# Kernel optimization log

Measured on AMD Instinct MI355X. Metric: run time of the kernel, lower is better.

## Reference

```python
import jax, jax.numpy as jnp
import numpy as np

B, S, D = 2, 2048, 1024
H, HD = 16, 64          # num_heads, head_dim
K = 32                  # JL n_components


def setup_inputs() -> dict:
    key = jax.random.key(0)
    k1, k2, k3, k4 = jax.random.split(key, 4)
    return {
        "hidden_states": jax.random.normal(k1, (B, S, D), dtype=jnp.float32),
        "W_attn": jax.random.normal(k2, (D, 3 * D), dtype=jnp.float32) * 0.02,
        "b_attn": jnp.zeros((3 * D,), dtype=jnp.float32),
        "S_proj": jax.random.normal(k3, (K, HD), dtype=jnp.float32) / np.sqrt(K),
        "W_proj": jax.random.normal(k4, (D, D), dtype=jnp.float32) * 0.02,
        "b_proj": jnp.zeros((D,), dtype=jnp.float32),
    }


def reference(hidden_states, W_attn, b_attn, S_proj, W_proj, b_proj):
    b, s, d = hidden_states.shape
    # GPT2 Conv1D: x @ W + b, then split into q,k,v
    qkv = hidden_states @ W_attn + b_attn            # [B,S,3D]
    q, k, v = jnp.split(qkv, 3, axis=-1)
    # split heads -> [B,H,S,HD]
    def split_heads(x):
        return x.reshape(b, s, H, HD).transpose(0, 2, 1, 3)
    q = split_heads(q) @ S_proj.T                    # [B,H,S,K] JL-reduced
    k = split_heads(k) @ S_proj.T                    # [B,H,S,K]
    v = split_heads(v)                               # [B,H,S,HD]
    # naive attention: scale by sqrt(value head_dim) per GPT2 _attn
    scores = jnp.einsum("bhqk,bhsk->bhqs", q, k) / jnp.sqrt(
        jnp.asarray(HD, dtype=v.dtype))              # [B,H,S,S]
    causal = jnp.tril(jnp.ones((s, s), dtype=bool))
    mask_value = jnp.finfo(scores.dtype).min
    scores = jnp.where(causal, scores, mask_value)
    attn = jax.nn.softmax(scores, axis=-1)
    out = jnp.einsum("bhqs,bhsd->bhqd", attn, v)     # [B,H,S,HD]
    out = out.transpose(0, 2, 1, 3).reshape(b, s, d)  # merge heads
    return out @ W_proj + b_proj
```

## Files before the change

### kernel.cpp

```cpp
#include <hip/hip_runtime.h>
#include <hip/hip_bf16.h>
#include <stdint.h>

#define B_ 2
#define S_ 2048
#define D_ 1024
#define H_ 16
#define HD_ 64
#define KJL 32
#define N3 3072
#define N2 2048

typedef __attribute__((ext_vector_type(8))) __bf16 bf16x8;
typedef __attribute__((ext_vector_type(4))) float floatx4;
typedef __attribute__((ext_vector_type(4))) short short4v;
typedef __attribute__((ext_vector_type(2))) unsigned int uint2v;

__device__ __forceinline__ unsigned short f2b(float x) {
  union { float f; unsigned u; } v; v.f = x;
  unsigned r = v.u + 0x7fffu + ((v.u >> 16) & 1u);
  return (unsigned short)(r >> 16);
}

__device__ __forceinline__ unsigned int pkbf(float lo, float hi) {
  union { float f; unsigned u; } a, b;
  a.f = lo; b.f = hi;
  return __builtin_amdgcn_perm(b.u + 0x8000u, a.u + 0x8000u, 0x07060302u);
}

__device__ __forceinline__ void async16(const void* g, void* l) {
  __builtin_amdgcn_global_load_lds((__attribute__((address_space(1))) void*)(g),
                                   (__attribute__((address_space(3))) void*)(l),
                                   16, 0, 0);
}

__global__ __launch_bounds__(256)
void prep_kernel(const float* __restrict__ hidden, unsigned short* __restrict__ hB,
                 const float* __restrict__ W_attn, const float* __restrict__ b_attn,
                 const float* __restrict__ Sp, const float* __restrict__ W_proj,
                 unsigned short* __restrict__ Bt2, unsigned short* __restrict__ WpT,
                 float* __restrict__ bias2) {
  __shared__ float shmem[2048];
  const int bid = blockIdx.x;
  const int tid = threadIdx.x;

  if (bid < 512) {
    const int n4 = (B_ * S_ * D_) / 4;
    int i = bid * 256 + tid;
    for (; i < n4; i += 512 * 256) {
      float4 v = *(const float4*)(hidden + 4 * (size_t)i);
      short4v o = {(short)f2b(v.x), (short)f2b(v.y), (short)f2b(v.z), (short)f2b(v.w)};
      *(short4v*)(hB + 4 * (size_t)i) = o;
    }
  } else if (bid < 2560) {
    const float* in;
    unsigned short* out;
    int Cs, local;
    if (bid < 1536) { local = bid - 512;  in = W_attn + 2048; out = Bt2 + 1024 * 1024; Cs = N3; }
    else            { local = bid - 1536; in = W_proj;        out = WpT;               Cs = D_; }
    float (*t)[33] = (float(*)[33])shmem;
    int c0 = (local & 31) * 32, r0 = (local >> 5) * 32;
    int tx = tid & 31, ty = tid >> 5;
    for (int j = 0; j < 32; j += 8)
      t[ty + j][tx] = in[(size_t)(r0 + ty + j) * Cs + c0 + tx];
    __syncthreads();
    for (int j = 0; j < 32; j += 8)
      out[(size_t)(c0 + ty + j) * D_ + r0 + tx] = f2b(t[tx][ty + j]);
  } else {
    const int lb = bid - 2560;
    const int part = lb >> 6;
    const int h = (lb >> 2) & 15;
    const int dc = lb & 3;
    for (int i = tid; i < 32 * 64; i += 256) shmem[i] = Sp[i];
    __syncthreads();
    const float scale = part ? 1.0f : 0.125f * 1.44269504f;
    const int d = dc * 256 + tid;
    float w[64];
    const float* src = W_attn + (size_t)d * N3 + part * D_ + h * 64;
    for (int j = 0; j < 16; ++j) {
      float4 v = *(const float4*)&src[j * 4];
      w[j * 4 + 0] = v.x; w[j * 4 + 1] = v.y; w[j * 4 + 2] = v.z; w[j * 4 + 3] = v.w;
    }
    const int nbase = part * 512 + h * 32;
    for (int kjl = 0; kjl < 32; ++kjl) {
      float acc = 0.f;
      for (int hd = 0; hd < 64; ++hd) acc += w[hd] * shmem[kjl * 64 + hd];
      Bt2[(size_t)(nbase + kjl) * D_ + d] = f2b(acc * scale);
    }
    if (dc == 0 && tid < 32) {
      float acc = 0.f;
      for (int hd = 0; hd < 64; ++hd) acc += b_attn[part * D_ + h * 64 + hd] * shmem[tid * 64 + hd];
      bias2[nbase + tid] = acc * scale;
    }
  }
}

__global__ __launch_bounds__(256, 2)
void qkv2_gemm_kernel(const unsigned short* __restrict__ A,
                      const unsigned short* __restrict__ Bt,
                      const float* __restrict__ b_attn,
                      const float* __restrict__ bias2,
                      unsigned short* __restrict__ Qjl,
                      unsigned short* __restrict__ Kjl,
                      unsigned short* __restrict__ Vc) {
  __shared__ __align__(16) unsigned short As[2][128 * 32];
  __shared__ __align__(16) unsigned short Bs[2][128 * 32];
  const int tid = threadIdx.x;
  const int lane = tid & 63, wv = tid >> 6;
  const int quad = lane >> 4, col = lane & 15;
  const int wm = wv >> 1, wn = wv & 1;
  const int m0 = blockIdx.y * 128, n0 = blockIdx.x * 128;

  floatx4 acc[4][4] = {};

  for (int kk = 0; kk < D_; kk += 64) {
    for (int it = 0; it < 4; ++it) {
      int c = it * 256 + tid;
      int ks = c >> 9, row = (c >> 2) & 127, kc = c & 3;
      async16(A + (size_t)(m0 + row) * D_ + kk + ks * 32 + kc * 8,
              (unsigned short*)As + c * 8);
    }
    for (int it = 0; it < 4; ++it) {
      int c = it * 256 + tid;
      int ks = c >> 9, row = (c >> 2) & 127, kc = c & 3;
      async16(Bt + (size_t)(n0 + row) * D_ + kk + ks * 32 + kc * 8,
              (unsigned short*)Bs + c * 8);
    }
    asm volatile("s_waitcnt vmcnt(0)" ::: "memory");
    __syncthreads();
    for (int ks = 0; ks < 2; ++ks) {
      bf16x8 af[4], bfr[4];
      for (int mt = 0; mt < 4; ++mt)
        af[mt] = *(const bf16x8*)&As[ks][(wm * 64 + mt * 16 + col) * 32 + quad * 8];
      for (int nt = 0; nt < 4; ++nt)
        bfr[nt] = *(const bf16x8*)&Bs[ks][(wn * 64 + nt * 16 + col) * 32 + quad * 8];
      for (int mt = 0; mt < 4; ++mt)
        for (int nt = 0; nt < 4; ++nt)
          acc[mt][nt] = __builtin_amdgcn_mfma_f32_16x16x32_bf16(
              af[mt], bfr[nt], acc[mt][nt], 0, 0, 0);
    }
    __syncthreads();
  }

  const int pq = n0 >> 9;
  for (int mt = 0; mt < 4; ++mt) {
    int gm0 = m0 + wm * 64 + mt * 16 + quad * 4;
    int b = gm0 >> 11, s = gm0 & (S_ - 1);
    for (int nt = 0; nt < 4; ++nt) {
      int gn = n0 + wn * 64 + nt * 16 + col;
      if (pq >= 2) {
        int vcol = gn - 1024;
        float bs = b_attn[2048 + vcol];
        int h = vcol >> 6, hd = vcol & 63;
        short4v vv;
        for (int i = 0; i < 4; ++i)
          vv[i] = (short)f2b(acc[mt][nt][i] + bs);
        size_t idx = ((((size_t)(b * H_ + h) * 64 + (s >> 5)) * 64 + hd) * 32 + (s & 31));
        *(short4v*)&Vc[idx] = vv;
      } else {
        float bs = bias2[gn];
        int gl = gn & 511;
        int h = gl >> 5, kjl = gl & 31;
        unsigned short* dst = pq ? Kjl : Qjl;
        size_t base = ((size_t)(b * H_ + h) * S_ + s) * KJL + kjl;
        for (int i = 0; i < 4; ++i)
          dst[base + (size_t)i * KJL] = f2b(acc[mt][nt][i] + bs);
      }
    }
  }
}

__global__ __launch_bounds__(512, 1)
void attn_kernel(const unsigned short* __restrict__ Qjl,
                 const unsigned short* __restrict__ Kjl,
                 const unsigned short* __restrict__ Vc,
                 unsigned short* __restrict__ AO) {
  __shared__ __align__(16) unsigned short Kb[3][4096];
  __shared__ __align__(16) unsigned short Vb[3][8192];
  __shared__ __align__(16) unsigned short Ps[8][2048];
  const int tid = threadIdx.x;
  const int lane = tid & 63, wv = tid >> 6;
  const int quad = lane >> 4, l15 = lane & 15;

  const int blk = blockIdx.x;
  const int bh = blk & 31;
  const int u = blk >> 5;
  const int b = bh >> 4, h = bh & 15;

  const unsigned short* Kg = Kjl + (size_t)bh * S_ * KJL;
  const unsigned short* Vg = Vc + (size_t)bh * (64 * 64 * 32);

  char* Pw = (char*)&Ps[wv][0];
  const int pswz = l15 << 4;
  const floatx4 zz = {0.f, 0.f, 0.f, 0.f};

#define STAGE(bu, c) do {                                                   \
    const char* ks_ = (const char*)(Kg + (size_t)(c) * 4096);               \
    const char* vs_ = (const char*)(Vg + (size_t)(c) * 8192);               \
    char* kd_ = (char*)&Kb[bu][0];                                          \
    char* vd_ = (char*)&Vb[bu][0];                                          \
    async16(ks_ + tid * 16,        kd_ + tid * 16);                         \
    async16(vs_ + tid * 16,        vd_ + tid * 16);                         \
    async16(vs_ + tid * 16 + 8192, vd_ + tid * 16 + 8192);                  \
  } while (0)

  for (int ph = 0; ph < 2; ++ph) {
    const int g = ph ? (15 - u) : u;
    const int t = g * 8 + wv;
    const int nch = g + 1;
    const int lastc = g;

    bf16x8 aq = *(const bf16x8*)&Qjl[(size_t)(bh * S_ + t * 16 + l15) * KJL + quad * 8];

    floatx4 o[4] = {};
    floatx4 psum = {};

    STAGE(0, 0);
    if (nch > 1) {
      STAGE(1, 1);
      asm volatile("s_waitcnt vmcnt(3)" ::: "memory");
    } else {
      asm volatile("s_waitcnt vmcnt(0)" ::: "memory");
    }
    __builtin_amdgcn_s_barrier();

    for (int kt = 0; kt < nch; ++kt) {
      const int cur = kt % 3;
      if (kt + 2 < nch) STAGE((kt + 2) % 3, kt + 2);

      const char* Kc = (const char*)&Kb[cur][0];
      const char* Vl = (const char*)&Vb[cur][0];

      bf16x8 ak[8];
      for (int sm = 0; sm < 8; ++sm)
        ak[sm] = *(const bf16x8*)(Kc + (sm * 16 + l15) * 64 + quad * 16);

      floatx4 sc[8];
      __builtin_amdgcn_s_setprio(1);
      for (int sm = 0; sm < 8; ++sm)
        sc[sm] = __builtin_amdgcn_mfma_f32_16x16x32_bf16(ak[sm], aq, zz, 0, 0, 0);
      __builtin_amdgcn_s_setprio(0);

      if (kt == lastc) {
        int qloc = wv * 16 + l15;
        for (int sm = 0; sm < 8; ++sm)
          for (int i = 0; i < 4; ++i)
            if (sm * 16 + quad * 4 + i > qloc) sc[sm][i] = -1e30f;
      }

      for (int sm = 0; sm < 8; ++sm) {
        float p0 = __builtin_amdgcn_exp2f(sc[sm][0]);
        float p1 = __builtin_amdgcn_exp2f(sc[sm][1]);
        float p2 = __builtin_amdgcn_exp2f(sc[sm][2]);
        float p3 = __builtin_amdgcn_exp2f(sc[sm][3]);
        psum[0] += p0; psum[1] += p1; psum[2] += p2; psum[3] += p3;
        uint2v pk2 = {pkbf(p0, p1), pkbf(p2, p3)};
        *(uint2v*)(Pw + l15 * 256 + ((sm * 32 + quad * 8) ^ pswz)) = pk2;
      }

      for (int ks = 0; ks < 4; ++ks) {
        bf16x8 bv[4];
        for (int md = 0; md < 4; ++md)
          bv[md] = *(const bf16x8*)(Vl + ks * 4096 + md * 1024 + l15 * 64 + quad * 16);
        bf16x8 bp = *(const bf16x8*)(Pw + l15 * 256 + ((ks * 64 + quad * 16) ^ pswz));
        __builtin_amdgcn_s_setprio(1);
        for (int md = 0; md < 4; ++md)
          o[md] = __builtin_amdgcn_mfma_f32_16x16x32_bf16(bv[md], bp, o[md], 0, 0, 0);
        __builtin_amdgcn_s_setprio(0);
      }

      if (kt + 2 < nch) {
        asm volatile("s_waitcnt vmcnt(3)" ::: "memory");
      } else {
        asm volatile("s_waitcnt vmcnt(0)" ::: "memory");
      }
      __builtin_amdgcn_s_barrier();
    }

    float l0 = psum[0] + psum[1] + psum[2] + psum[3];
    l0 += __shfl_xor(l0, 16, 64);
    l0 += __shfl_xor(l0, 32, 64);
    float inv = 1.f / l0;

    {
      const int eswz = (l15 & 7) << 4;
      for (int md = 0; md < 4; ++md) {
        uint2v t4 = {pkbf(o[md][0] * inv, o[md][1] * inv),
                     pkbf(o[md][2] * inv, o[md][3] * inv)};
        *(uint2v*)(Pw + l15 * 128 + ((md * 32 + quad * 8) ^ eswz)) = t4;
      }
      asm volatile("s_waitcnt lgkmcnt(0)" ::: "memory");
      int q = lane >> 2, j = lane & 3;
      size_t gbase = ((size_t)(b * S_ + t * 16 + q)) * D_ + h * HD_;
      for (int half = 0; half < 2; ++half) {
        bf16x8 v = *(const bf16x8*)(Pw + q * 128 + ((half * 64 + j * 16) ^ ((q & 7) << 4)));
        *(bf16x8*)&AO[gbase + half * 32 + j * 8] = v;
      }
    }
  }
#undef STAGE
}

__global__ __launch_bounds__(256, 2)
void proj_gemm_kernel(const unsigned short* __restrict__ A,
                      const unsigned short* __restrict__ Bt,
                      const float* __restrict__ bias,
                      float* __restrict__ out) {
  __shared__ __align__(16) unsigned short As[2][64 * 32];
  __shared__ __align__(16) unsigned short Bs[2][128 * 32];
  const int tid = threadIdx.x;
  const int lane = tid & 63, wv = tid >> 6;
  const int quad = lane >> 4, col = lane & 15;
  const int wm = wv >> 1, wn = wv & 1;
  const int m0 = blockIdx.y * 64, n0 = blockIdx.x * 128;

  floatx4 acc[2][4] = {};

  for (int kk = 0; kk < D_; kk += 64) {
    for (int it = 0; it < 2; ++it) {
      int c = it * 256 + tid;
      int ks = c >> 8, row = (c >> 2) & 63, kc = c & 3;
      async16(A + (size_t)(m0 + row) * D_ + kk + ks * 32 + kc * 8,
              (unsigned short*)As + c * 8);
    }
    for (int it = 0; it < 4; ++it) {
      int c = it * 256 + tid;
      int ks = c >> 9, row = (c >> 2) & 127, kc = c & 3;
      async16(Bt + (size_t)(n0 + row) * D_ + kk + ks * 32 + kc * 8,
              (unsigned short*)Bs + c * 8);
    }
    asm volatile("s_waitcnt vmcnt(0)" ::: "memory");
    __syncthreads();
    for (int ks = 0; ks < 2; ++ks) {
      bf16x8 af[2], bfr[4];
      for (int mt = 0; mt < 2; ++mt)
        af[mt] = *(const bf16x8*)&As[ks][(wm * 32 + mt * 16 + col) * 32 + quad * 8];
      for (int nt = 0; nt < 4; ++nt)
        bfr[nt] = *(const bf16x8*)&Bs[ks][(wn * 64 + nt * 16 + col) * 32 + quad * 8];
      for (int mt = 0; mt < 2; ++mt)
        for (int nt = 0; nt < 4; ++nt)
          acc[mt][nt] = __builtin_amdgcn_mfma_f32_16x16x32_bf16(
              af[mt], bfr[nt], acc[mt][nt], 0, 0, 0);
    }
    __syncthreads();
  }

  for (int mt = 0; mt < 2; ++mt) {
    int gm0 = m0 + wm * 32 + mt * 16 + quad * 4;
    for (int nt = 0; nt < 4; ++nt) {
      int gn = n0 + wn * 64 + nt * 16 + col;
      float bs = bias[gn];
      for (int i = 0; i < 4; ++i)
        out[(size_t)(gm0 + i) * D_ + gn] = acc[mt][nt][i] + bs;
    }
  }
}

extern "C" void kernel_launch(void* const* d_in, const int* in_sizes, int n_in,
                              void* d_out, int out_size, void* d_ws, size_t ws_size,
                              hipStream_t stream) {
  (void)in_sizes; (void)n_in; (void)out_size; (void)ws_size;
  const float* hidden = (const float*)d_in[0];
  const float* W_attn = (const float*)d_in[1];
  const float* b_attn = (const float*)d_in[2];
  const float* S_proj = (const float*)d_in[3];
  const float* W_proj = (const float*)d_in[4];
  const float* b_proj = (const float*)d_in[5];
  float* out = (float*)d_out;

  char* ws = (char*)d_ws;
  unsigned short* hB    = (unsigned short*)(ws);
  unsigned short* Bt2   = (unsigned short*)(ws + (8u << 20));
  unsigned short* WpT   = (unsigned short*)(ws + (12u << 20));
  float*          bias2 = (float*)         (ws + (14u << 20));
  unsigned short* Qjl   = (unsigned short*)(ws + (15u << 20));
  unsigned short* Kjl   = (unsigned short*)(ws + (19u << 20));
  unsigned short* Vc    = (unsigned short*)(ws + (23u << 20));
  unsigned short* AO    = (unsigned short*)(ws + (31u << 20));

  prep_kernel<<<2688, 256, 0, stream>>>(hidden, hB, W_attn, b_attn, S_proj,
                                        W_proj, Bt2, WpT, bias2);
  qkv2_gemm_kernel<<<dim3(N2 / 128, (B_ * S_) / 128), 256, 0, stream>>>(
      hB, Bt2, b_attn, bias2, Qjl, Kjl, Vc);
  attn_kernel<<<256, 512, 0, stream>>>(Qjl, Kjl, Vc, AO);
  proj_gemm_kernel<<<dim3(D_ / 128, (B_ * S_) / 64), 256, 0, stream>>>(
      AO, WpT, b_proj, out);
}
```

Before: 179.2 us.

## Split attention blocks into 256-thread 64-query tiles with double buffering

The attention kernel now runs 512 blocks of 4 waves, each covering 64 query rows instead of 128, with two blocks allowed per CU. The K/V staging drops from triple to double buffering with a full vmcnt(0) wait each iteration, and each thread issues twice as many async copies. The aim is finer work granularity and better occupancy and load balance across CUs. In exchange, each K/V chunk is loaded by twice as many blocks and the shallower pipeline exposes more memory latency.

```diff
diff --git a/kernel.cpp b/kernel.cpp
--- a/kernel.cpp
+++ b/kernel.cpp
@@ -170,21 +170,21 @@
   }
 }
 
-__global__ __launch_bounds__(512, 1)
+__global__ __launch_bounds__(256, 2)
 void attn_kernel(const unsigned short* __restrict__ Qjl,
                  const unsigned short* __restrict__ Kjl,
                  const unsigned short* __restrict__ Vc,
                  unsigned short* __restrict__ AO) {
-  __shared__ __align__(16) unsigned short Kb[3][4096];
-  __shared__ __align__(16) unsigned short Vb[3][8192];
-  __shared__ __align__(16) unsigned short Ps[8][2048];
+  __shared__ __align__(16) unsigned short Kb[2][4096];
+  __shared__ __align__(16) unsigned short Vb[2][8192];
+  __shared__ __align__(16) unsigned short Ps[4][2048];
   const int tid = threadIdx.x;
   const int lane = tid & 63, wv = tid >> 6;
   const int quad = lane >> 4, l15 = lane & 15;
 
   const int blk = blockIdx.x;
   const int bh = blk & 31;
-  const int u = blk >> 5;
+  const int v = blk >> 5;
   const int b = bh >> 4, h = bh & 15;
 
   const unsigned short* Kg = Kjl + (size_t)bh * S_ * KJL;
@@ -199,34 +199,33 @@
     const char* vs_ = (const char*)(Vg + (size_t)(c) * 8192);               \
     char* kd_ = (char*)&Kb[bu][0];                                          \
     char* vd_ = (char*)&Vb[bu][0];                                          \
-    async16(ks_ + tid * 16,        kd_ + tid * 16);                         \
-    async16(vs_ + tid * 16,        vd_ + tid * 16);                         \
-    async16(vs_ + tid * 16 + 8192, vd_ + tid * 16 + 8192);                  \
+    async16(ks_ + tid * 16,         kd_ + tid * 16);                        \
+    async16(ks_ + tid * 16 + 4096,  kd_ + tid * 16 + 4096);                 \
+    async16(vs_ + tid * 16,         vd_ + tid * 16);                        \
+    async16(vs_ + tid * 16 + 4096,  vd_ + tid * 16 + 4096);                 \
+    async16(vs_ + tid * 16 + 8192,  vd_ + tid * 16 + 8192);                 \
+    async16(vs_ + tid * 16 + 12288, vd_ + tid * 16 + 12288);                \
   } while (0)
 
   for (int ph = 0; ph < 2; ++ph) {
-    const int g = ph ? (15 - u) : u;
-    const int t = g * 8 + wv;
-    const int nch = g + 1;
-    const int lastc = g;
-
-    bf16x8 aq = *(const bf16x8*)&Qjl[(size_t)(bh * S_ + t * 16 + l15) * KJL + quad * 8];
+    const int gv = ph ? (31 - v) : v;
+    const int t16 = gv * 4 + wv;
+    const int nch = (gv >> 1) + 1;
+    const int lastc = nch - 1;
+    const int qbase = (gv & 1) * 64 + wv * 16;
+
+    bf16x8 aq = *(const bf16x8*)&Qjl[(size_t)(bh * S_ + t16 * 16 + l15) * KJL + quad * 8];
 
     floatx4 o[4] = {};
     floatx4 psum = {};
 
     STAGE(0, 0);
-    if (nch > 1) {
-      STAGE(1, 1);
-      asm volatile("s_waitcnt vmcnt(3)" ::: "memory");
-    } else {
-      asm volatile("s_waitcnt vmcnt(0)" ::: "memory");
-    }
+    asm volatile("s_waitcnt vmcnt(0)" ::: "memory");
     __builtin_amdgcn_s_barrier();
 
+    int cur = 0;
     for (int kt = 0; kt < nch; ++kt) {
-      const int cur = kt % 3;
-      if (kt + 2 < nch) STAGE((kt + 2) % 3, kt + 2);
+      if (kt + 1 < nch) STAGE(cur ^ 1, kt + 1);
 
       const char* Kc = (const char*)&Kb[cur][0];
       const char* Vl = (const char*)&Vb[cur][0];
@@ -242,7 +241,7 @@
       __builtin_amdgcn_s_setprio(0);
 
       if (kt == lastc) {
-        int qloc = wv * 16 + l15;
+        int qloc = qbase + l15;
         for (int sm = 0; sm < 8; ++sm)
           for (int i = 0; i < 4; ++i)
             if (sm * 16 + quad * 4 + i > qloc) sc[sm][i] = -1e30f;
@@ -269,12 +268,9 @@
         __builtin_amdgcn_s_setprio(0);
       }
 
-      if (kt + 2 < nch) {
-        asm volatile("s_waitcnt vmcnt(3)" ::: "memory");
-      } else {
-        asm volatile("s_waitcnt vmcnt(0)" ::: "memory");
-      }
+      asm volatile("s_waitcnt vmcnt(0)" ::: "memory");
       __builtin_amdgcn_s_barrier();
+      cur ^= 1;
     }
 
     float l0 = psum[0] + psum[1] + psum[2] + psum[3];
@@ -291,10 +287,10 @@
       }
       asm volatile("s_waitcnt lgkmcnt(0)" ::: "memory");
       int q = lane >> 2, j = lane & 3;
-      size_t gbase = ((size_t)(b * S_ + t * 16 + q)) * D_ + h * HD_;
+      size_t gbase = ((size_t)(b * S_ + t16 * 16 + q)) * D_ + h * HD_;
       for (int half = 0; half < 2; ++half) {
-        bf16x8 v = *(const bf16x8*)(Pw + q * 128 + ((half * 64 + j * 16) ^ ((q & 7) << 4)));
-        *(bf16x8*)&AO[gbase + half * 32 + j * 8] = v;
+        bf16x8 vv = *(const bf16x8*)(Pw + q * 128 + ((half * 64 + j * 16) ^ ((q & 7) << 4)));
+        *(bf16x8*)&AO[gbase + half * 32 + j * 8] = vv;
       }
     }
   }
@@ -382,7 +378,7 @@
                                         W_proj, Bt2, WpT, bias2);
   qkv2_gemm_kernel<<<dim3(N2 / 128, (B_ * S_) / 128), 256, 0, stream>>>(
       hB, Bt2, b_attn, bias2, Qjl, Kjl, Vc);
-  attn_kernel<<<256, 512, 0, stream>>>(Qjl, Kjl, Vc, AO);
+  attn_kernel<<<512, 256, 0, stream>>>(Qjl, Kjl, Vc, AO);
   proj_gemm_kernel<<<dim3(D_ / 128, (B_ * S_) / 64), 256, 0, stream>>>(
       AO, WpT, b_proj, out);
 }
```

After: 178.1 us, median of 2. About the same (-0.6%).
